# Kernel optimization log

Measured on AMD Instinct MI355X. Metric: run time of the kernel, lower is better.

The kernel has to match this reference:

```python
import jax, jax.numpy as jnp
import numpy as np

ALPHA = 0.2  # LeakyReLU negative slope
NEG_INF = -9e15


def setup_inputs() -> dict:
    key = jax.random.key(0)
    k_h, k_adj, k_W, k_a = jax.random.split(key, 4)
    B, N, Din, Dout = 8, 1024, 256, 256
    h = jax.random.normal(k_h, (B, N, Din), dtype=jnp.float32)
    adj = jax.random.randint(k_adj, (B, N, N), 0, 2, dtype=jnp.int32)
    # nn.Linear weight [out, in], xavier-uniform-ish init for a
    W = jax.random.normal(k_W, (Dout, Din), dtype=jnp.float32) * (1.0 / np.sqrt(Din))
    lim = np.float32(1.414 * np.sqrt(6.0 / (2 * Dout + 1)))
    a = jax.random.uniform(k_a, (2 * Dout, 1), dtype=jnp.float32, minval=-lim, maxval=lim)
    return {"h": h, "adj": adj, "W": W, "a": a}


def reference(h, adj, W, a):
    # Wh: [B, N, F]
    Wh = jnp.einsum('bnd,fd->bnf', h, W)
    F_ = Wh.shape[-1]
    # Decompose concat-then-matmul: e_ij = leakyrelu(Wh_i @ a1 + Wh_j @ a2)
    a1 = a[:F_, 0]   # [F]
    a2 = a[F_:, 0]   # [F]
    src = Wh @ a1    # [B, N]  score contribution of row node i
    dst = Wh @ a2    # [B, N]  score contribution of col node j
    e = src[:, :, None] + dst[:, None, :]          # [B, N, N]
    e = jnp.where(e > 0, e, ALPHA * e)             # LeakyReLU
    e = jnp.where(adj > 0, e, NEG_INF)             # mask non-edges
    attention = jax.nn.softmax(e, axis=-1)         # [B, N, N]
    # dropout p=0.0 -> identity in eval/train
    h_prime = jnp.einsum('bij,bjf->bif', attention, Wh)
    return h_prime
```

## Files before the change

kernel.cpp:

```cpp
#include <hip/hip_runtime.h>
#include <hip/hip_bf16.h>
#include <cstdint>

#define ALPHA 0.2f
#define NEG_INF -9000000000000000.0f

typedef __bf16 bf16_t;
typedef __bf16 bf16x8 __attribute__((ext_vector_type(8)));
typedef float f32x16 __attribute__((ext_vector_type(16)));

__global__ __launch_bounds__(256) void k_pre(
    const float* __restrict__ h, const float* __restrict__ W, const float* __restrict__ a,
    const int* __restrict__ adj, bf16_t* __restrict__ WhT,
    float* __restrict__ src, float* __restrict__ dst,
    unsigned long long* __restrict__ mask_ws)
{
  __shared__ __align__(16) char smem[64 * 72 * 2 * sizeof(bf16_t)];
  const int bx = blockIdx.x;
  const int t = threadIdx.x;

  if (bx < 512) {
    bf16_t* WS = (bf16_t*)smem;
    bf16_t* HS = WS + 64 * 72;
    const int b  = bx & 7;
    const int jt = (bx >> 3) & 15;
    const int ft = bx >> 7;
    const int j0 = jt * 64, f0 = ft * 64;
    const int w = t >> 6, lane = t & 63;
    const int mrow = lane & 31, half = lane >> 5;
    const int fsub = (w & 1) * 32, jsub = (w >> 1) * 32;

    const int lr = t >> 2;
    const int lc = (t & 3) * 16;
    const float* wp = W + ((size_t)(f0 + lr)) * 256 + lc;
    const float* hp = h + ((size_t)(b * 1024 + j0 + lr)) * 256 + lc;

    f32x16 acc;
#pragma unroll
    for (int r = 0; r < 16; r++) acc[r] = 0.f;

    for (int s = 0; s < 4; s++) {
      if (s) __syncthreads();
      {
        float4 w0 = *(const float4*)(wp + s * 64);
        float4 w1 = *(const float4*)(wp + s * 64 + 4);
        float4 w2 = *(const float4*)(wp + s * 64 + 8);
        float4 w3 = *(const float4*)(wp + s * 64 + 12);
        bf16x8 va, vb;
        va[0] = (bf16_t)w0.x; va[1] = (bf16_t)w0.y; va[2] = (bf16_t)w0.z; va[3] = (bf16_t)w0.w;
        va[4] = (bf16_t)w1.x; va[5] = (bf16_t)w1.y; va[6] = (bf16_t)w1.z; va[7] = (bf16_t)w1.w;
        vb[0] = (bf16_t)w2.x; vb[1] = (bf16_t)w2.y; vb[2] = (bf16_t)w2.z; vb[3] = (bf16_t)w2.w;
        vb[4] = (bf16_t)w3.x; vb[5] = (bf16_t)w3.y; vb[6] = (bf16_t)w3.z; vb[7] = (bf16_t)w3.w;
        *(bf16x8*)&WS[lr * 72 + lc] = va;
        *(bf16x8*)&WS[lr * 72 + lc + 8] = vb;
        float4 h0 = *(const float4*)(hp + s * 64);
        float4 h1 = *(const float4*)(hp + s * 64 + 4);
        float4 h2 = *(const float4*)(hp + s * 64 + 8);
        float4 h3 = *(const float4*)(hp + s * 64 + 12);
        bf16x8 vc, vd;
        vc[0] = (bf16_t)h0.x; vc[1] = (bf16_t)h0.y; vc[2] = (bf16_t)h0.z; vc[3] = (bf16_t)h0.w;
        vc[4] = (bf16_t)h1.x; vc[5] = (bf16_t)h1.y; vc[6] = (bf16_t)h1.z; vc[7] = (bf16_t)h1.w;
        vd[0] = (bf16_t)h2.x; vd[1] = (bf16_t)h2.y; vd[2] = (bf16_t)h2.z; vd[3] = (bf16_t)h2.w;
        vd[4] = (bf16_t)h3.x; vd[5] = (bf16_t)h3.y; vd[6] = (bf16_t)h3.z; vd[7] = (bf16_t)h3.w;
        *(bf16x8*)&HS[lr * 72 + lc] = vc;
        *(bf16x8*)&HS[lr * 72 + lc + 8] = vd;
      }
      __syncthreads();
#pragma unroll
      for (int ks = 0; ks < 4; ks++) {
        bf16x8 af = *(const bf16x8*)&WS[(fsub + mrow) * 72 + ks * 16 + half * 8];
        bf16x8 bf = *(const bf16x8*)&HS[(jsub + mrow) * 72 + ks * 16 + half * 8];
        acc = __builtin_amdgcn_mfma_f32_32x32x16_bf16(af, bf, acc, 0, 0, 0);
      }
    }

    const int jcol = j0 + jsub + mrow;
#pragma unroll
    for (int r = 0; r < 16; r++) {
      int frow = fsub + (r & 3) + 8 * (r >> 2) + 4 * half;
      WhT[(((size_t)(b * 256 + f0 + frow)) << 10) + jcol] = (bf16_t)acc[r];
    }
  } else {
    float* uS = (float*)smem;
    const int p  = bx - 512;
    const int m0 = p * 16;
    {
      float s1a = 0.f, s1b = 0.f, s2a = 0.f, s2b = 0.f;
#pragma unroll 4
      for (int f = 0; f < 256; f += 2) {
        float w0 = W[f * 256 + t];
        float w1 = W[(f + 1) * 256 + t];
        s1a = fmaf(w0, a[f], s1a);       s1b = fmaf(w1, a[f + 1], s1b);
        s2a = fmaf(w0, a[256 + f], s2a); s2b = fmaf(w1, a[256 + f + 1], s2b);
      }
      uS[t] = s1a + s1b; uS[256 + t] = s2a + s2b;
    }
    __syncthreads();
    {
      const int n = t >> 4, c = t & 15;
      const int m = m0 + n;
      const float* hp = h + (size_t)m * 256 + c * 16;
      float s1 = 0.f, s2 = 0.f;
#pragma unroll
      for (int i = 0; i < 4; i++) {
        float4 v = *(const float4*)(hp + i * 4);
        const float* u1p = &uS[c * 16 + i * 4];
        const float* u2p = &uS[256 + c * 16 + i * 4];
        s1 = fmaf(v.x, u1p[0], s1); s1 = fmaf(v.y, u1p[1], s1);
        s1 = fmaf(v.z, u1p[2], s1); s1 = fmaf(v.w, u1p[3], s1);
        s2 = fmaf(v.x, u2p[0], s2); s2 = fmaf(v.y, u2p[1], s2);
        s2 = fmaf(v.z, u2p[2], s2); s2 = fmaf(v.w, u2p[3], s2);
      }
#pragma unroll
      for (int off = 8; off; off >>= 1) {
        s1 += __shfl_down(s1, off, 16);
        s2 += __shfl_down(s2, off, 16);
      }
      if (c == 0) { src[m] = s1; dst[m] = s2; }
    }
    {
      const int wv = t >> 6, lane = t & 63;
#pragma unroll 4
      for (int r = 0; r < 16; r++) {
        const size_t row = (size_t)(m0 + r);
        const int4 av = *(const int4*)(adj + (row << 10) + 4 * t);
        unsigned long long b0 = __ballot(av.x > 0);
        unsigned long long b1 = __ballot(av.y > 0);
        unsigned long long b2 = __ballot(av.z > 0);
        unsigned long long b3 = __ballot(av.w > 0);
        if (lane == 0) {
          unsigned long long* mp = mask_ws + row * 16 + wv * 4;
          mp[0] = b0; mp[1] = b1; mp[2] = b2; mp[3] = b3;
        }
      }
    }
  }
}

__global__ __launch_bounds__(512) void k_attn(
    const bf16_t* __restrict__ WhT, const float* __restrict__ src, const float* __restrict__ dst,
    const unsigned long long* __restrict__ mask_ws, float* __restrict__ out)
{
  const int b  = blockIdx.x & 7;
  const int i0 = (blockIdx.x >> 3) << 5;
  const int t  = threadIdx.x;
  const int w  = t >> 6;
  const int lane = t & 63;
  const int mrow = lane & 31, half = lane >> 5;

  __shared__ float dstE[1024], dstF[1024];
  __shared__ float srcE[32], srcF[32];
  __shared__ unsigned long long maskS[32 * 16];
  __shared__ bf16_t P[2][32 * 264];

  {
    float2 d2 = *(const float2*)(dst + (b << 10) + t * 2);
    dstE[t * 2]     = __expf(d2.x);  dstF[t * 2]     = __expf(ALPHA * d2.x);
    dstE[t * 2 + 1] = __expf(d2.y);  dstF[t * 2 + 1] = __expf(ALPHA * d2.y);
  }
  if (t < 32) {
    float s = src[(b << 10) + i0 + t];
    srcE[t] = __expf(s);  srcF[t] = __expf(ALPHA * s);
  }
  maskS[t] = mask_ws[((size_t)(b << 10) + i0) * 16 + t];
  __syncthreads();

  f32x16 acc, acc2;
#pragma unroll
  for (int r = 0; r < 16; r++) { acc[r] = 0.f; acc2[r] = 0.f; }

  bf16x8 ones;
#pragma unroll
  for (int k = 0; k < 8; k++) ones[k] = (bf16_t)1.0f;

  const bf16_t* bp = WhT + (((size_t)(b * 256 + w * 32 + mrow)) << 10);
  const int jj = t & 255, ih = t >> 8;

  for (int c = 0; c < 4; c++) {
    bf16_t* Pc = &P[c & 1][0];
    {
      float Edj = dstE[c * 256 + jj];
      float Fdj = dstF[c * 256 + jj];
      int mi = c * 4 + (jj & 3);
      int sh = jj >> 2;
#pragma unroll
      for (int r = 0; r < 16; r++) {
        int i = ih * 16 + r;
        unsigned long long w64 = maskS[i * 16 + mi];
        float pp = srcE[i] * Edj;
        float pn = srcF[i] * Fdj;
        float p = (pp > 1.0f) ? pp : pn;
        p = ((w64 >> sh) & 1ull) ? p : 0.0f;
        Pc[i * 264 + jj] = (bf16_t)p;
      }
    }
    __syncthreads();

    const bf16_t* bpc = bp + c * 256 + half * 8;
    const bf16_t* prow = Pc + mrow * 264 + half * 8;
#pragma unroll
    for (int idx = 0; idx < 16; idx++) {
      bf16x8 afr = *(const bf16x8*)(prow + idx * 16);
      bf16x8 bfr = *(const bf16x8*)(bpc + idx * 16);
      acc  = __builtin_amdgcn_mfma_f32_32x32x16_bf16(afr, bfr, acc, 0, 0, 0);
      acc2 = __builtin_amdgcn_mfma_f32_32x32x16_bf16(afr, ones, acc2, 0, 0, 0);
    }
  }

  const int col = w * 32 + mrow;
#pragma unroll
  for (int r = 0; r < 16; r++) {
    int row = (r & 3) + 8 * (r >> 2) + 4 * half;
    out[((size_t)(b << 10) + i0 + row) * 256 + col] = acc[r] / acc2[r];
  }
}

extern "C" void kernel_launch(void* const* d_in, const int* in_sizes, int n_in,
                              void* d_out, int out_size, void* d_ws, size_t ws_size,
                              hipStream_t stream) {
  const float* h   = (const float*)d_in[0];
  const int*   adj = (const int*)d_in[1];
  const float* W   = (const float*)d_in[2];
  const float* a   = (const float*)d_in[3];
  float* out = (float*)d_out;

  char* wsb = (char*)d_ws;
  bf16_t* WhT = (bf16_t*)wsb;
  float* srcv = (float*)(wsb + (4u << 20));
  float* dstv = srcv + 8192;
  unsigned long long* mask_ws = (unsigned long long*)(wsb + (4u << 20) + 65536);

  k_pre <<<1024, 256, 0, stream>>>(h, W, a, adj, WhT, srcv, dstv, mask_ws);
  k_attn<<<256,  512, 0, stream>>>(WhT, srcv, dstv, mask_ws, out);
}
```

Measured before the change: 119.2 us.

## Drop row-sum MFMA, compute softmax denominators on VALU, precompute exponentials

The second MFMA that multiplied P by a ones vector to get row sums is removed. Row sums are now accumulated in registers while P is built, reduced through shared memory, and applied as a reciprocal. Exponentials of src and dst are moved into the pre-kernel, and the mask bit layout is changed so each thread writes 16 contiguous P entries with vector stores. This halves the MFMA work in the attention kernel and cuts shared-memory traffic, at the cost of extra barriers and a small fp32 reduction. The adj loads become scalar int loads instead of int4.

Measured after the change: 121.3 us. About the same (+1.7%).

```diff
diff --git a/kernel.cpp b/kernel.cpp
--- a/kernel.cpp
+++ b/kernel.cpp
@@ -3,7 +3,6 @@
 #include <cstdint>
 
 #define ALPHA 0.2f
-#define NEG_INF -9000000000000000.0f
 
 typedef __bf16 bf16_t;
 typedef __bf16 bf16x8 __attribute__((ext_vector_type(8)));
@@ -12,7 +11,8 @@
 __global__ __launch_bounds__(256) void k_pre(
     const float* __restrict__ h, const float* __restrict__ W, const float* __restrict__ a,
     const int* __restrict__ adj, bf16_t* __restrict__ WhT,
-    float* __restrict__ src, float* __restrict__ dst,
+    float* __restrict__ srcE, float* __restrict__ srcF,
+    float* __restrict__ dstE, float* __restrict__ dstF,
     unsigned long long* __restrict__ mask_ws)
 {
   __shared__ __align__(16) char smem[64 * 72 * 2 * sizeof(bf16_t)];
@@ -116,21 +116,24 @@
         s1 += __shfl_down(s1, off, 16);
         s2 += __shfl_down(s2, off, 16);
       }
-      if (c == 0) { src[m] = s1; dst[m] = s2; }
+      if (c == 0) {
+        srcE[m] = __expf(s1); srcF[m] = __expf(ALPHA * s1);
+        dstE[m] = __expf(s2); dstF[m] = __expf(ALPHA * s2);
+      }
     }
     {
       const int wv = t >> 6, lane = t & 63;
 #pragma unroll 4
       for (int r = 0; r < 16; r++) {
         const size_t row = (size_t)(m0 + r);
-        const int4 av = *(const int4*)(adj + (row << 10) + 4 * t);
-        unsigned long long b0 = __ballot(av.x > 0);
-        unsigned long long b1 = __ballot(av.y > 0);
-        unsigned long long b2 = __ballot(av.z > 0);
-        unsigned long long b3 = __ballot(av.w > 0);
+        const int* ap = adj + (row << 10) + t;
+        unsigned long long b0 = __ballot(ap[0] > 0);
+        unsigned long long b1 = __ballot(ap[256] > 0);
+        unsigned long long b2 = __ballot(ap[512] > 0);
+        unsigned long long b3 = __ballot(ap[768] > 0);
         if (lane == 0) {
-          unsigned long long* mp = mask_ws + row * 16 + wv * 4;
-          mp[0] = b0; mp[1] = b1; mp[2] = b2; mp[3] = b3;
+          unsigned long long* mp = mask_ws + row * 16 + wv;
+          mp[0] = b0; mp[4] = b1; mp[8] = b2; mp[12] = b3;
         }
       }
     }
@@ -138,7 +141,9 @@
 }
 
 __global__ __launch_bounds__(512) void k_attn(
-    const bf16_t* __restrict__ WhT, const float* __restrict__ src, const float* __restrict__ dst,
+    const bf16_t* __restrict__ WhT,
+    const float* __restrict__ srcEg, const float* __restrict__ srcFg,
+    const float* __restrict__ dstEg, const float* __restrict__ dstFg,
     const unsigned long long* __restrict__ mask_ws, float* __restrict__ out)
 {
   const int b  = blockIdx.x & 7;
@@ -147,52 +152,65 @@
   const int w  = t >> 6;
   const int lane = t & 63;
   const int mrow = lane & 31, half = lane >> 5;
-
-  __shared__ float dstE[1024], dstF[1024];
-  __shared__ float srcE[32], srcF[32];
+  const int ip = t & 31;
+  const int g  = t >> 5;
+
+  __shared__ float dstE_s[1024], dstF_s[1024];
   __shared__ unsigned long long maskS[32 * 16];
   __shared__ bf16_t P[2][32 * 264];
-
-  {
-    float2 d2 = *(const float2*)(dst + (b << 10) + t * 2);
-    dstE[t * 2]     = __expf(d2.x);  dstF[t * 2]     = __expf(ALPHA * d2.x);
-    dstE[t * 2 + 1] = __expf(d2.y);  dstF[t * 2 + 1] = __expf(ALPHA * d2.y);
-  }
-  if (t < 32) {
-    float s = src[(b << 10) + i0 + t];
-    srcE[t] = __expf(s);  srcF[t] = __expf(ALPHA * s);
-  }
-  maskS[t] = mask_ws[((size_t)(b << 10) + i0) * 16 + t];
+  __shared__ float rsS[512];
+  __shared__ float rowRcp[32];
+
+  if (t < 256) {
+    float4 v = *(const float4*)(dstEg + (b << 10) + t * 4);
+    *(float4*)&dstE_s[t * 4] = v;
+  } else {
+    float4 v = *(const float4*)(dstFg + (b << 10) + (t - 256) * 4);
+    *(float4*)&dstF_s[(t - 256) * 4] = v;
+  }
+  maskS[t] = mask_ws[((size_t)((b << 10) + i0)) * 16 + t];
+  const float srcEi = srcEg[(b << 10) + i0 + ip];
+  const float srcFi = srcFg[(b << 10) + i0 + ip];
   __syncthreads();
 
-  f32x16 acc, acc2;
-#pragma unroll
-  for (int r = 0; r < 16; r++) { acc[r] = 0.f; acc2[r] = 0.f; }
-
-  bf16x8 ones;
-#pragma unroll
-  for (int k = 0; k < 8; k++) ones[k] = (bf16_t)1.0f;
+  unsigned long long mw[4];
+#pragma unroll
+  for (int c = 0; c < 4; c++) mw[c] = maskS[ip * 16 + 4 * c + (g >> 2)];
+  const int sh = (g & 3) * 16;
+
+  f32x16 acc;
+#pragma unroll
+  for (int r = 0; r < 16; r++) acc[r] = 0.f;
+  float rsA = 0.f, rsB = 0.f;
 
   const bf16_t* bp = WhT + (((size_t)(b * 256 + w * 32 + mrow)) << 10);
-  const int jj = t & 255, ih = t >> 8;
-
+
+#pragma unroll
   for (int c = 0; c < 4; c++) {
     bf16_t* Pc = &P[c & 1][0];
     {
-      float Edj = dstE[c * 256 + jj];
-      float Fdj = dstF[c * 256 + jj];
-      int mi = c * 4 + (jj & 3);
-      int sh = jj >> 2;
-#pragma unroll
-      for (int r = 0; r < 16; r++) {
-        int i = ih * 16 + r;
-        unsigned long long w64 = maskS[i * 16 + mi];
-        float pp = srcE[i] * Edj;
-        float pn = srcF[i] * Fdj;
-        float p = (pp > 1.0f) ? pp : pn;
-        p = ((w64 >> sh) & 1ull) ? p : 0.0f;
-        Pc[i * 264 + jj] = (bf16_t)p;
-      }
+      unsigned int m16 = (unsigned int)(mw[c] >> sh);
+      float ev[16], fv[16];
+      const float* dE = &dstE_s[c * 256 + g * 16];
+      const float* dF = &dstF_s[c * 256 + g * 16];
+#pragma unroll
+      for (int q = 0; q < 4; q++) {
+        *(float4*)&ev[q * 4] = *(const float4*)(dE + q * 4);
+        *(float4*)&fv[q * 4] = *(const float4*)(dF + q * 4);
+      }
+      bf16x8 v0, v1;
+#pragma unroll
+      for (int k = 0; k < 16; k++) {
+        float pp = srcEi * ev[k];
+        float pn = srcFi * fv[k];
+        float pv = (pp > 1.0f) ? pp : pn;
+        pv = (m16 & (1u << k)) ? pv : 0.0f;
+        if (k & 1) rsB += pv; else rsA += pv;
+        bf16_t pb = (bf16_t)pv;
+        if (k < 8) v0[k] = pb; else v1[k - 8] = pb;
+      }
+      *(bf16x8*)&Pc[ip * 264 + g * 16] = v0;
+      *(bf16x8*)&Pc[ip * 264 + g * 16 + 8] = v1;
     }
     __syncthreads();
 
@@ -202,16 +220,25 @@
     for (int idx = 0; idx < 16; idx++) {
       bf16x8 afr = *(const bf16x8*)(prow + idx * 16);
       bf16x8 bfr = *(const bf16x8*)(bpc + idx * 16);
-      acc  = __builtin_amdgcn_mfma_f32_32x32x16_bf16(afr, bfr, acc, 0, 0, 0);
-      acc2 = __builtin_amdgcn_mfma_f32_32x32x16_bf16(afr, ones, acc2, 0, 0, 0);
-    }
-  }
+      acc = __builtin_amdgcn_mfma_f32_32x32x16_bf16(afr, bfr, acc, 0, 0, 0);
+    }
+  }
+
+  rsS[g * 32 + ip] = rsA + rsB;
+  __syncthreads();
+  if (t < 32) {
+    float s = 0.f;
+#pragma unroll
+    for (int gg = 0; gg < 16; gg++) s += rsS[gg * 32 + t];
+    rowRcp[t] = 1.0f / s;
+  }
+  __syncthreads();
 
   const int col = w * 32 + mrow;
 #pragma unroll
   for (int r = 0; r < 16; r++) {
     int row = (r & 3) + 8 * (r >> 2) + 4 * half;
-    out[((size_t)(b << 10) + i0 + row) * 256 + col] = acc[r] / acc2[r];
+    out[((size_t)((b << 10) + i0 + row)) * 256 + col] = acc[r] * rowRcp[row];
   }
 }
 
@@ -226,10 +253,12 @@
 
   char* wsb = (char*)d_ws;
   bf16_t* WhT = (bf16_t*)wsb;
-  float* srcv = (float*)(wsb + (4u << 20));
-  float* dstv = srcv + 8192;
-  unsigned long long* mask_ws = (unsigned long long*)(wsb + (4u << 20) + 65536);
-
-  k_pre <<<1024, 256, 0, stream>>>(h, W, a, adj, WhT, srcv, dstv, mask_ws);
-  k_attn<<<256,  512, 0, stream>>>(WhT, srcv, dstv, mask_ws, out);
+  float* srcE = (float*)(wsb + (4u << 20));
+  float* srcF = srcE + 8192;
+  float* dstE = srcF + 8192;
+  float* dstF = dstE + 8192;
+  unsigned long long* mask_ws = (unsigned long long*)(wsb + (4u << 20) + 131072);
+
+  k_pre <<<1024, 256, 0, stream>>>(h, W, a, adj, WhT, srcE, srcF, dstE, dstF, mask_ws);
+  k_attn<<<256,  512, 0, stream>>>(WhT, srcE, srcF, dstE, dstF, mask_ws, out);
 }
```
